# Kernel optimization log

Measured on AMD Instinct MI355X. Metric: run time of the kernel, lower is better.

The kernel has to match this reference:

```python
import jax, jax.numpy as jnp
import numpy as np

N_QUESTIONS = 2000
N_CATS = 4
MEMORY_SIZE = 50
KEY_DIM = 50
VALUE_DIM = 200
FINAL_FC = 50
ABILITY_SCALE = 3.0
BATCH = 1024
SEQ_LEN = 500


def setup_inputs() -> dict:
    key = jax.random.key(0)
    ks = jax.random.split(key, 20)
    f32 = jnp.float32
    inp = {}
    # integer data: question ids in [1, n_questions], responses in [0, K)
    inp['q_data'] = jax.random.randint(ks[0], (BATCH, SEQ_LEN), 1, N_QUESTIONS + 1)
    inp['r_data'] = jax.random.randint(ks[1], (BATCH, SEQ_LEN), 0, N_CATS)
    s = 0.05
    inp['q_embed_w'] = jax.random.normal(ks[2], (N_QUESTIONS + 1, KEY_DIM), f32) * s
    inp['Mk'] = jax.random.normal(ks[3], (MEMORY_SIZE, KEY_DIM), f32) * s
    inp['Mv0'] = jax.random.normal(ks[4], (MEMORY_SIZE, VALUE_DIM), f32) * s
    inp['Wv'] = jax.random.normal(ks[5], (VALUE_DIM, N_CATS * N_QUESTIONS), f32) * s
    inp['bv'] = jnp.zeros((VALUE_DIM,), f32)
    # DKVMN erase / add transforms
    inp['We'] = jax.random.normal(ks[6], (VALUE_DIM, VALUE_DIM), f32) * s
    inp['be'] = jnp.zeros((VALUE_DIM,), f32)
    inp['Wa'] = jax.random.normal(ks[7], (VALUE_DIM, VALUE_DIM), f32) * s
    inp['ba'] = jnp.zeros((VALUE_DIM,), f32)
    # summary network
    inp['Ws'] = jax.random.normal(ks[8], (FINAL_FC, VALUE_DIM + KEY_DIM), f32) * s
    inp['bs'] = jnp.zeros((FINAL_FC,), f32)
    # ability / threshold / discrimination heads
    inp['Wth'] = jax.random.normal(ks[9], (1, FINAL_FC), f32) * s
    inp['bth'] = jnp.zeros((1,), f32)
    inp['Wbeta'] = jax.random.normal(ks[10], (N_CATS - 1, KEY_DIM), f32) * s
    inp['bbeta'] = jnp.zeros((N_CATS - 1,), f32)
    inp['Wdisc'] = jax.random.normal(ks[11], (1, FINAL_FC + KEY_DIM), f32) * s
    inp['bdisc'] = jnp.zeros((1,), f32)
    return inp


def _deep_gpcm(q_data, r_data, q_embed_w, Mk, Mv0, Wv, bv, We, be, Wa, ba,
               Ws, bs, Wth, bth, Wbeta, bbeta, Wdisc, bdisc):
    B, S = q_data.shape
    K = Wbeta.shape[0] + 1
    D = Wv.shape[0]
    Q = Wv.shape[1] // K
    # view gpcm_value_embed weight as (D, K, Q): one-hot(q) @ W == gather column q
    WvK = Wv.reshape(D, K, Q)
    k_idx = jnp.arange(K, dtype=jnp.float32)
    Mv_init = jnp.broadcast_to(Mv0[None], (B,) + Mv0.shape)

    def step(Mv, inp):
        q_t, r_t = inp  # (B,), (B,)
        qe = q_embed_w[q_t]  # (B, key_dim)
        # linear decay weights: max(0, 1 - |k - r| / (K-1))
        w = jnp.maximum(0.0, 1.0 - jnp.abs(k_idx[None, :] - r_t[:, None].astype(jnp.float32)) / (K - 1))  # (B, K)
        Wvq = jnp.take(WvK, q_t - 1, axis=2)  # (D, K, B)
        ve = jnp.einsum('dkb,bk->bd', Wvq, w) + bv  # value embedding (B, D)
        # DKVMN attention + read
        cw = jax.nn.softmax(qe @ Mk.T, axis=-1)  # (B, mem)
        read = jnp.einsum('bm,bmd->bd', cw, Mv)
        # summary / IRT heads
        summary = jnp.tanh(jnp.concatenate([read, qe], axis=-1) @ Ws.T + bs)  # (B, fc)
        theta = ABILITY_SCALE * (summary @ Wth.T + bth)[:, 0]  # (B,)
        betas = jnp.tanh(qe @ Wbeta.T + bbeta)  # (B, K-1)
        alpha = jax.nn.softplus(jnp.concatenate([summary, qe], axis=-1) @ Wdisc.T + bdisc)[:, 0]  # (B,)
        # erase-add memory write
        erase = jax.nn.sigmoid(ve @ We.T + be)
        add = jnp.tanh(ve @ Wa.T + ba)
        Mv_new = Mv * (1.0 - cw[:, :, None] * erase[:, None, :]) + cw[:, :, None] * add[:, None, :]
        # GPCM cumulative logits -> softmax
        cum = jnp.cumsum(alpha[:, None] * (theta[:, None] - betas), axis=-1)  # (B, K-1)
        logits = jnp.concatenate([jnp.zeros((B, 1), cum.dtype), cum], axis=-1)  # (B, K)
        probs = jax.nn.softmax(logits, axis=-1)
        return Mv_new, probs

    _, probs = jax.lax.scan(step, Mv_init, (q_data.T, r_data.T))  # (S, B, K)
    return jnp.transpose(probs, (1, 0, 2))  # (B, S, K)


def reference(q_data, r_data, q_embed_w, Mk, Mv0, Wv, bv, We, be, Wa, ba,
              Ws, bs, Wth, bth, Wbeta, bbeta, Wdisc, bdisc):
    return _deep_gpcm(q_data, r_data, q_embed_w, Mk, Mv0, Wv, bv, We, be, Wa, ba,
                      Ws, bs, Wth, bth, Wbeta, bbeta, Wdisc, bdisc)
```

## Files before the change

kernel.cpp:

```cpp
#include <hip/hip_runtime.h>
#include <hip/hip_bf16.h>
#include <cstdint>
#include <cstddef>


namespace {
constexpr int kB   = 1024;
constexpr int kS   = 500;
constexpr int kQ   = 2000;
constexpr int kKD  = 50;
constexpr int kMem = 50;
constexpr int kD   = 200;
constexpr int kFC  = 50;
constexpr int kWP  = 216;

constexpr size_t OFF_EAD  = 0;
constexpr size_t OFF_CW   = OFF_EAD + (size_t)kQ * 4 * kD * 2;
constexpr size_t OFF_SQ   = OFF_CW + 100064;
constexpr size_t OFF_BQ   = OFF_SQ + 100064;
constexpr size_t OFF_DQ   = OFF_BQ + 8032;
constexpr size_t OFF_CE   = OFF_DQ + 2016;
constexpr size_t OFF_CA   = OFF_CE + 224;
constexpr size_t OFF_WET  = OFF_CA + 224;
constexpr size_t OFF_WAT  = OFF_WET + 40000;
}

typedef float f32x2 __attribute__((ext_vector_type(2)));
typedef _Float16 h2_t __attribute__((ext_vector_type(2)));

__device__ __forceinline__ f32x2 pk_fma(f32x2 a, f32x2 b, f32x2 c) {
  f32x2 d;
  asm("v_pk_fma_f32 %0, %1, %2, %3" : "=v"(d) : "v"(a), "v"(b), "v"(c));
  return d;
}

__device__ __forceinline__ void lds_barrier() {
  asm volatile("s_waitcnt lgkmcnt(0)" ::: "memory");
  __builtin_amdgcn_s_barrier();
  asm volatile("" ::: "memory");
}

__device__ __forceinline__ float fast_tanh(float x) {
  const float ax = fabsf(x);
  const float t = __expf(-2.f * ax);
  const float r = (1.f - t) / (1.f + t);
  return copysignf(r, x);
}
__device__ __forceinline__ float fast_softplus(float x) {
  return fmaxf(x, 0.f) + log1pf(__expf(-fabsf(x)));
}

__global__ void prep1_misc(const float* __restrict__ We, const float* __restrict__ Wa,
                           const float* __restrict__ bv, const float* __restrict__ be,
                           const float* __restrict__ ba, float* __restrict__ ws) {
  float* WeT = ws + OFF_WET;
  float* WaT = ws + OFF_WAT;
  float* ce  = ws + OFF_CE;
  float* ca  = ws + OFF_CA;
  const int gt = blockIdx.x * 256 + threadIdx.x;
  const int stride = gridDim.x * 256;
  for (int e = gt; e < kD * kD; e += stride) {
    const int i = e / kD;
    const int dd = e - i * kD;
    WeT[e] = We[dd * kD + i];
    WaT[e] = Wa[dd * kD + i];
  }
  for (int dd = gt; dd < kD; dd += stride) {
    float acc_e = be[dd], acc_a = ba[dd];
    for (int i = 0; i < kD; ++i) {
      acc_e = fmaf(We[dd * kD + i], bv[i], acc_e);
      acc_a = fmaf(Wa[dd * kD + i], bv[i], acc_a);
    }
    ce[dd] = acc_e;
    ca[dd] = acc_a;
  }
}

__global__ void prep2_ead(const float* __restrict__ Wv, float* __restrict__ ws) {
  __shared__ float s_wv[4][kD];
  const int tid = threadIdx.x;
  const int qm1 = blockIdx.x;
  for (int e = tid; e < 4 * kD; e += 256) {
    const int k = e / kD;
    const int i = e - k * kD;
    s_wv[k][i] = Wv[(size_t)i * (4 * kQ) + (size_t)k * kQ + qm1];
  }
  __syncthreads();
  const int d = tid;
  if (d < kD) {
    const float* WeT = ws + OFF_WET;
    const float* WaT = ws + OFF_WAT;
    float e0 = 0.f, e1 = 0.f, e2 = 0.f, e3 = 0.f;
    float a0 = 0.f, a1 = 0.f, a2 = 0.f, a3 = 0.f;
    for (int i = 0; i < kD; ++i) {
      const float we = WeT[i * kD + d];
      const float wa = WaT[i * kD + d];
      e0 = fmaf(we, s_wv[0][i], e0);
      e1 = fmaf(we, s_wv[1][i], e1);
      e2 = fmaf(we, s_wv[2][i], e2);
      e3 = fmaf(we, s_wv[3][i], e3);
      a0 = fmaf(wa, s_wv[0][i], a0);
      a1 = fmaf(wa, s_wv[1][i], a1);
      a2 = fmaf(wa, s_wv[2][i], a2);
      a3 = fmaf(wa, s_wv[3][i], a3);
    }
    const float ced = ws[OFF_CE + d];
    const float cad = ws[OFF_CA + d];
    const float W[4][4] = {{1.f, 2.f / 3.f, 1.f / 3.f, 0.f},
                           {2.f / 3.f, 1.f, 2.f / 3.f, 1.f / 3.f},
                           {1.f / 3.f, 2.f / 3.f, 1.f, 2.f / 3.f},
                           {0.f, 1.f / 3.f, 2.f / 3.f, 1.f}};
#pragma unroll
    for (int r = 0; r < 4; ++r) {
      const float ep = ced + W[r][0] * e0 + W[r][1] * e1 + W[r][2] * e2 + W[r][3] * e3;
      const float ap = cad + W[r][0] * a0 + W[r][1] * a1 + W[r][2] * a2 + W[r][3] * a3;
      float2 v;
      v.x = 1.f / (1.f + expf(-ep));
      v.y = tanhf(ap);
      *reinterpret_cast<float2*>(ws + OFF_EAD + ((size_t)(qm1 * 4 + r) * kD + d) * 2) = v;
    }
  }
}

__global__ void prep3_qtables(const float* __restrict__ q_embed_w, const float* __restrict__ Mk,
                              const float* __restrict__ Ws, const float* __restrict__ bs,
                              const float* __restrict__ Wbeta, const float* __restrict__ bbeta,
                              const float* __restrict__ Wdisc, float* __restrict__ ws) {
  __shared__ float s_qe[kKD];
  const int tid = threadIdx.x;
  const int q = blockIdx.x;
  if (tid < kKD) s_qe[tid] = q_embed_w[q * kKD + tid];
  __syncthreads();
  {
    float s = -1e30f;
    if (tid < kMem) {
      s = 0.f;
      for (int j = 0; j < kKD; ++j) s = fmaf(s_qe[j], Mk[tid * kKD + j], s);
    }
    float mx = s;
#pragma unroll
    for (int o = 1; o < 64; o <<= 1) mx = fmaxf(mx, __shfl_xor(mx, o));
    const float ev = (tid < kMem) ? expf(s - mx) : 0.f;
    float sm = ev;
#pragma unroll
    for (int o = 1; o < 64; o <<= 1) sm += __shfl_xor(sm, o);
    if (tid < kMem) ws[OFF_CW + (size_t)q * kMem + tid] = ev / sm;
  }
  if (tid < kFC) {
    float s = bs[tid];
    for (int j = 0; j < kKD; ++j) s = fmaf(s_qe[j], Ws[tid * 250 + kD + j], s);
    ws[OFF_SQ + (size_t)q * kFC + tid] = s;
  }
  if (tid < 4) {
    float v = 0.f;
    if (tid < 3) {
      float s = bbeta[tid];
      for (int j = 0; j < kKD; ++j) s = fmaf(s_qe[j], Wbeta[tid * kKD + j], s);
      v = tanhf(s);
    }
    ws[OFF_BQ + (size_t)q * 4 + tid] = v;
  }
  if (tid == 0) {
    float s = 0.f;
    for (int j = 0; j < kKD; ++j) s = fmaf(s_qe[j], Wdisc[kFC + j], s);
    ws[OFF_DQ + q] = s;
  }
}

__device__ __forceinline__ void do_finale(int l, float wth_f, float wds_f, float bth0,
                                          float bdisc0, const float (*s_part)[64],
                                          const float* s_sq_row, const float* s_bqdq_row,
                                          float* out_ptr) {
  float summ = 0.f;
  if (l < kFC) {
    const float sp = s_part[0][l] + s_part[1][l] + s_part[2][l] + s_part[3][l] +
                     s_part[4][l] + s_sq_row[l];
    summ = fast_tanh(sp);
  }
  float p1 = wth_f * summ;
  float p2 = wds_f * summ;
#pragma unroll
  for (int o = 1; o < 64; o <<= 1) {
    p1 += __shfl_xor(p1, o);
    p2 += __shfl_xor(p2, o);
  }
  if (l == 0) {
    const float theta = 3.f * (p1 + bth0);
    const float alpha = fast_softplus(p2 + s_bqdq_row[3] + bdisc0);
    const float c1 = alpha * (theta - s_bqdq_row[0]);
    const float c2 = c1 + alpha * (theta - s_bqdq_row[1]);
    const float c3 = c2 + alpha * (theta - s_bqdq_row[2]);
    const float mx = fmaxf(fmaxf(0.f, c1), fmaxf(c2, c3));
    const float x0 = __expf(0.f - mx);
    const float x1 = __expf(c1 - mx);
    const float x2 = __expf(c2 - mx);
    const float x3 = __expf(c3 - mx);
    const float inv = 1.f / (x0 + x1 + x2 + x3);
    float4 pr;
    pr.x = x0 * inv;
    pr.y = x1 * inv;
    pr.z = x2 * inv;
    pr.w = x3 * inv;
    *reinterpret_cast<float4*>(out_ptr) = pr;
  }
}

__launch_bounds__(256, 4)
__global__ void dkvmn_main(const int* __restrict__ q_data, const int* __restrict__ r_data,
                           const float* __restrict__ Mv0, const float* __restrict__ Ws,
                           const float* __restrict__ Wth, const float* __restrict__ bth,
                           const float* __restrict__ Wdisc, const float* __restrict__ bdisc,
                           const float* __restrict__ ws, float* __restrict__ out) {
  const int tid = threadIdx.x;
  const int b = blockIdx.x;
  const int lane = tid & 63;
  const int wid = tid >> 6;
  const float* EAD = ws + OFF_EAD;
  const float* CW = ws + OFF_CW;
  const float* SQ = ws + OFF_SQ;
  const float* BQ = ws + OFF_BQ;
  const float* DQ = ws + OFF_DQ;

  __shared__ __align__(16) _Float16 s_wsh[kFC * kWP];
  __shared__ __align__(16) _Float16 s_readh[208];
  __shared__ __align__(16) float s_cw[64];
  __shared__ float s_part[5][64];
  __shared__ float s_sq[2][kFC];
  __shared__ float s_bqdq[2][4];
  __shared__ int s_q[kS];
  __shared__ int s_qr[kS];

  for (int e = tid; e < kFC * kD; e += 256) {
    const int f = e / kD;
    const int dd = e - f * kD;
    s_wsh[f * kWP + dd] = (_Float16)Ws[f * 250 + dd];
  }
  {
    const int* qrow = q_data + (size_t)b * kS;
    const int* rrow = r_data + (size_t)b * kS;
    for (int e = tid; e < kS; e += 256) {
      const int qv = qrow[e];
      s_q[e] = qv;
      s_qr[e] = (qv - 1) * 4 + rrow[e];
    }
  }
  f32x2 mv[25];
  const int d = tid;
  const bool dact = (d < kD);
  if (dact) {
#pragma unroll
    for (int m = 0; m < 25; ++m) {
      mv[m][0] = Mv0[(2 * m) * kD + d];
      mv[m][1] = Mv0[(2 * m + 1) * kD + d];
    }
  }
  float wth_f = 0.f, wds_f = 0.f;
  if (wid == 3 && lane < kFC) {
    wth_f = Wth[lane];
    wds_f = Wdisc[lane];
  }
  const float bth0 = bth[0];
  const float bdisc0 = bdisc[0];
  float* out_b = out + (size_t)b * kS * 4;
  __syncthreads();

  const int q0 = s_q[0];
  const int qr0 = s_qr[0];
  float2 ea_cur = make_float2(0.f, 0.f);
  if (dact) ea_cur = *reinterpret_cast<const float2*>(EAD + ((size_t)qr0 * kD + d) * 2);
  float cw_cur = 0.f;
  if (wid == 1 && lane < kMem) cw_cur = CW[(size_t)q0 * kMem + lane];
  float v2_cur = 0.f;
  if (wid == 2) {
    if (lane < kFC) v2_cur = SQ[(size_t)q0 * kFC + lane];
    else if (lane < 53) v2_cur = BQ[(size_t)q0 * 4 + (lane - 50)];
    else if (lane == 53) v2_cur = DQ[q0];
  }

  for (int t = 0; t < kS; ++t) {
    const int pb = t & 1;
    const int tn = (t + 1 < kS) ? (t + 1) : t;
    const int qn = s_q[tn];
    const int qrn = s_qr[tn];
    f32x2 en2 = {0.f, 0.f}, ad2 = {0.f, 0.f};
    float2 ea_nxt = ea_cur;
    if (dact) {
      ea_nxt = *reinterpret_cast<const float2*>(EAD + ((size_t)qrn * kD + d) * 2);
      en2[0] = -ea_cur.x;
      en2[1] = -ea_cur.x;
      ad2[0] = ea_cur.y;
      ad2[1] = ea_cur.y;
    }
    if (wid == 1) {
      if (lane < kMem) {
        s_cw[lane] = cw_cur;
        cw_cur = CW[(size_t)qn * kMem + lane];
      }
    }
    if (wid == 2) {
      if (lane < kFC) {
        s_sq[pb][lane] = v2_cur;
        v2_cur = SQ[(size_t)qn * kFC + lane];
      } else if (lane < 53) {
        s_bqdq[pb][lane - 50] = v2_cur;
        v2_cur = BQ[(size_t)qn * 4 + (lane - 50)];
      } else if (lane == 53) {
        s_bqdq[pb][3] = v2_cur;
        v2_cur = DQ[qn];
      }
    }
    lds_barrier();
    if (dact) {
      f32x2 r2a = {0.f, 0.f}, r2b = {0.f, 0.f};
      const float4* cw4 = reinterpret_cast<const float4*>(s_cw);
#pragma unroll
      for (int g = 0; g < 12; ++g) {
        const float4 c4 = cw4[g];
        const f32x2 clo = {c4.x, c4.y};
        const f32x2 chi = {c4.z, c4.w};
        r2a = pk_fma(clo, mv[2 * g], r2a);
        mv[2 * g] = pk_fma(clo, pk_fma(mv[2 * g], en2, ad2), mv[2 * g]);
        r2b = pk_fma(chi, mv[2 * g + 1], r2b);
        mv[2 * g + 1] = pk_fma(chi, pk_fma(mv[2 * g + 1], en2, ad2), mv[2 * g + 1]);
      }
      {
        const f32x2 clast = *reinterpret_cast<const f32x2*>(&s_cw[48]);
        r2a = pk_fma(clast, mv[24], r2a);
        mv[24] = pk_fma(clast, pk_fma(mv[24], en2, ad2), mv[24]);
      }
      s_readh[d] = (_Float16)((r2a[0] + r2b[0]) + (r2a[1] + r2b[1]));
    }
    if (wid == 3 && t > 0) {
      do_finale(lane, wth_f, wds_f, bth0, bdisc0, s_part, s_sq[pb ^ 1], s_bqdq[pb ^ 1],
                out_b + (size_t)(t - 1) * 4);
    }
    lds_barrier();
    if (tid < 250) {
      const int pc = tid / 50;
      const int pf = tid - pc * 50;
      const float4* wp = reinterpret_cast<const float4*>(s_wsh + pf * kWP + pc * 40);
      const float4* rp = reinterpret_cast<const float4*>(s_readh + pc * 40);
      float acc0 = 0.f, acc1 = 0.f;
#pragma unroll
      for (int g = 0; g < 5; ++g) {
        const float4 wv = wp[g];
        const float4 rv = rp[g];
        acc0 = __builtin_amdgcn_fdot2(__builtin_bit_cast(h2_t, wv.x),
                                      __builtin_bit_cast(h2_t, rv.x), acc0, false);
        acc1 = __builtin_amdgcn_fdot2(__builtin_bit_cast(h2_t, wv.y),
                                      __builtin_bit_cast(h2_t, rv.y), acc1, false);
        acc0 = __builtin_amdgcn_fdot2(__builtin_bit_cast(h2_t, wv.z),
                                      __builtin_bit_cast(h2_t, rv.z), acc0, false);
        acc1 = __builtin_amdgcn_fdot2(__builtin_bit_cast(h2_t, wv.w),
                                      __builtin_bit_cast(h2_t, rv.w), acc1, false);
      }
      s_part[pc][pf] = acc0 + acc1;
    }
    ea_cur = ea_nxt;
  }
  __syncthreads();
  if (wid == 3) {
    do_finale(lane, wth_f, wds_f, bth0, bdisc0, s_part, s_sq[(kS - 1) & 1],
              s_bqdq[(kS - 1) & 1], out_b + (size_t)(kS - 1) * 4);
  }
}

extern "C" void kernel_launch(void* const* d_in, const int* in_sizes, int n_in,
                              void* d_out, int out_size, void* d_ws, size_t ws_size,
                              hipStream_t stream) {
  (void)in_sizes; (void)n_in; (void)out_size; (void)ws_size;
  const int* q_data = (const int*)d_in[0];
  const int* r_data = (const int*)d_in[1];
  const float* q_embed_w = (const float*)d_in[2];
  const float* Mk = (const float*)d_in[3];
  const float* Mv0 = (const float*)d_in[4];
  const float* Wv = (const float*)d_in[5];
  const float* bv = (const float*)d_in[6];
  const float* We = (const float*)d_in[7];
  const float* be = (const float*)d_in[8];
  const float* Wa = (const float*)d_in[9];
  const float* ba = (const float*)d_in[10];
  const float* Ws = (const float*)d_in[11];
  const float* bs = (const float*)d_in[12];
  const float* Wth = (const float*)d_in[13];
  const float* bth = (const float*)d_in[14];
  const float* Wbeta = (const float*)d_in[15];
  const float* bbeta = (const float*)d_in[16];
  const float* Wdisc = (const float*)d_in[17];
  const float* bdisc = (const float*)d_in[18];
  float* out = (float*)d_out;
  float* ws = (float*)d_ws;

  hipLaunchKernelGGL(prep1_misc, dim3(64), dim3(256), 0, stream, We, Wa, bv, be, ba, ws);
  hipLaunchKernelGGL(prep2_ead, dim3(kQ), dim3(256), 0, stream, Wv, ws);
  hipLaunchKernelGGL(prep3_qtables, dim3(kQ + 1), dim3(64), 0, stream, q_embed_w, Mk, Ws, bs,
                     Wbeta, bbeta, Wdisc, ws);
  hipLaunchKernelGGL(dkvmn_main, dim3(kB), dim3(256), 0, stream, q_data, r_data, Mv0, Ws, Wth,
                     bth, Wdisc, bdisc, ws, out);
}
```

Before: 1.389 ms.

## Software-pipeline recurrence stages to use one barrier per timestep

Restructures the per-timestep loop into a three-stage software pipeline. The memory read/update for step t, the summary dot products for step t-1, and the finale for step t-2 run concurrently, using double-buffered cw/read/partial arrays and triple-buffered per-question summary data. This removes one of the two LDS barriers per step, cutting synchronization on the sequential critical path. In exchange it adds an epilogue to drain the pipeline, more shared memory, and more complex buffer index bookkeeping.

```diff
diff --git a/kernel.cpp b/kernel.cpp
--- a/kernel.cpp
+++ b/kernel.cpp
@@ -222,11 +222,11 @@
   const float* DQ = ws + OFF_DQ;
 
   __shared__ __align__(16) _Float16 s_wsh[kFC * kWP];
-  __shared__ __align__(16) _Float16 s_readh[208];
-  __shared__ __align__(16) float s_cw[64];
-  __shared__ float s_part[5][64];
-  __shared__ float s_sq[2][kFC];
-  __shared__ float s_bqdq[2][4];
+  __shared__ __align__(16) _Float16 s_readh[2][208];
+  __shared__ __align__(16) float s_cw[2][64];
+  __shared__ float s_part[2][5][64];
+  __shared__ float s_sq[3][52];
+  __shared__ float s_bqdq[3][4];
   __shared__ int s_q[kS];
   __shared__ int s_qr[kS];
 
@@ -265,54 +265,57 @@
   __syncthreads();
 
   const int q0 = s_q[0];
-  const int qr0 = s_qr[0];
+  const int q1 = s_q[1];
   float2 ea_cur = make_float2(0.f, 0.f);
-  if (dact) ea_cur = *reinterpret_cast<const float2*>(EAD + ((size_t)qr0 * kD + d) * 2);
+  if (dact) ea_cur = *reinterpret_cast<const float2*>(EAD + ((size_t)s_qr[0] * kD + d) * 2);
   float cw_cur = 0.f;
-  if (wid == 1 && lane < kMem) cw_cur = CW[(size_t)q0 * kMem + lane];
+  if (wid == 1 && lane < kMem) {
+    s_cw[0][lane] = CW[(size_t)q0 * kMem + lane];
+    cw_cur = CW[(size_t)q1 * kMem + lane];
+  }
   float v2_cur = 0.f;
   if (wid == 2) {
     if (lane < kFC) v2_cur = SQ[(size_t)q0 * kFC + lane];
     else if (lane < 53) v2_cur = BQ[(size_t)q0 * 4 + (lane - 50)];
     else if (lane == 53) v2_cur = DQ[q0];
   }
-
+  __syncthreads();
+
+  int i3 = 0;
   for (int t = 0; t < kS; ++t) {
     const int pb = t & 1;
-    const int tn = (t + 1 < kS) ? (t + 1) : t;
-    const int qn = s_q[tn];
-    const int qrn = s_qr[tn];
+    const int ip1 = (i3 + 1 < 3) ? i3 + 1 : 0;
+    const int tn1 = (t + 1 < kS) ? t + 1 : kS - 1;
+    const int tn2 = (t + 2 < kS) ? t + 2 : kS - 1;
     f32x2 en2 = {0.f, 0.f}, ad2 = {0.f, 0.f};
     float2 ea_nxt = ea_cur;
     if (dact) {
-      ea_nxt = *reinterpret_cast<const float2*>(EAD + ((size_t)qrn * kD + d) * 2);
+      ea_nxt = *reinterpret_cast<const float2*>(EAD + ((size_t)s_qr[tn1] * kD + d) * 2);
       en2[0] = -ea_cur.x;
       en2[1] = -ea_cur.x;
       ad2[0] = ea_cur.y;
       ad2[1] = ea_cur.y;
     }
-    if (wid == 1) {
-      if (lane < kMem) {
-        s_cw[lane] = cw_cur;
-        cw_cur = CW[(size_t)qn * kMem + lane];
-      }
+    if (wid == 1 && lane < kMem) {
+      s_cw[pb ^ 1][lane] = cw_cur;
+      cw_cur = CW[(size_t)s_q[tn2] * kMem + lane];
     }
     if (wid == 2) {
+      const int qn = s_q[tn1];
       if (lane < kFC) {
-        s_sq[pb][lane] = v2_cur;
+        s_sq[i3][lane] = v2_cur;
         v2_cur = SQ[(size_t)qn * kFC + lane];
       } else if (lane < 53) {
-        s_bqdq[pb][lane - 50] = v2_cur;
+        s_bqdq[i3][lane - 50] = v2_cur;
         v2_cur = BQ[(size_t)qn * 4 + (lane - 50)];
       } else if (lane == 53) {
-        s_bqdq[pb][3] = v2_cur;
+        s_bqdq[i3][3] = v2_cur;
         v2_cur = DQ[qn];
       }
     }
-    lds_barrier();
     if (dact) {
       f32x2 r2a = {0.f, 0.f}, r2b = {0.f, 0.f};
-      const float4* cw4 = reinterpret_cast<const float4*>(s_cw);
+      const float4* cw4 = reinterpret_cast<const float4*>(s_cw[pb]);
 #pragma unroll
       for (int g = 0; g < 12; ++g) {
         const float4 c4 = cw4[g];
@@ -324,22 +327,21 @@
         mv[2 * g + 1] = pk_fma(chi, pk_fma(mv[2 * g + 1], en2, ad2), mv[2 * g + 1]);
       }
       {
-        const f32x2 clast = *reinterpret_cast<const f32x2*>(&s_cw[48]);
+        const f32x2 clast = *reinterpret_cast<const f32x2*>(&s_cw[pb][48]);
         r2a = pk_fma(clast, mv[24], r2a);
         mv[24] = pk_fma(clast, pk_fma(mv[24], en2, ad2), mv[24]);
       }
-      s_readh[d] = (_Float16)((r2a[0] + r2b[0]) + (r2a[1] + r2b[1]));
-    }
-    if (wid == 3 && t > 0) {
-      do_finale(lane, wth_f, wds_f, bth0, bdisc0, s_part, s_sq[pb ^ 1], s_bqdq[pb ^ 1],
-                out_b + (size_t)(t - 1) * 4);
-    }
-    lds_barrier();
+      s_readh[pb][d] = (_Float16)((r2a[0] + r2b[0]) + (r2a[1] + r2b[1]));
+    }
+    if (wid == 3 && t >= 2) {
+      do_finale(lane, wth_f, wds_f, bth0, bdisc0, s_part[pb ^ 1], s_sq[ip1], s_bqdq[ip1],
+                out_b + (size_t)(t - 2) * 4);
+    }
     if (tid < 250) {
       const int pc = tid / 50;
       const int pf = tid - pc * 50;
       const float4* wp = reinterpret_cast<const float4*>(s_wsh + pf * kWP + pc * 40);
-      const float4* rp = reinterpret_cast<const float4*>(s_readh + pc * 40);
+      const float4* rp = reinterpret_cast<const float4*>(&s_readh[pb ^ 1][pc * 40]);
       float acc0 = 0.f, acc1 = 0.f;
 #pragma unroll
       for (int g = 0; g < 5; ++g) {
@@ -354,14 +356,46 @@
         acc1 = __builtin_amdgcn_fdot2(__builtin_bit_cast(h2_t, wv.w),
                                       __builtin_bit_cast(h2_t, rv.w), acc1, false);
       }
-      s_part[pc][pf] = acc0 + acc1;
-    }
+      s_part[pb][pc][pf] = acc0 + acc1;
+    }
+    lds_barrier();
     ea_cur = ea_nxt;
-  }
-  __syncthreads();
-  if (wid == 3) {
-    do_finale(lane, wth_f, wds_f, bth0, bdisc0, s_part, s_sq[(kS - 1) & 1],
-              s_bqdq[(kS - 1) & 1], out_b + (size_t)(kS - 1) * 4);
+    i3 = ip1;
+  }
+  {
+    constexpr int pbE = kS & 1;
+    constexpr int i3a = (kS - 2) % 3;
+    constexpr int i3b = (kS - 1) % 3;
+    if (tid < 250) {
+      const int pc = tid / 50;
+      const int pf = tid - pc * 50;
+      const float4* wp = reinterpret_cast<const float4*>(s_wsh + pf * kWP + pc * 40);
+      const float4* rp = reinterpret_cast<const float4*>(&s_readh[(kS - 1) & 1][pc * 40]);
+      float acc0 = 0.f, acc1 = 0.f;
+#pragma unroll
+      for (int g = 0; g < 5; ++g) {
+        const float4 wv = wp[g];
+        const float4 rv = rp[g];
+        acc0 = __builtin_amdgcn_fdot2(__builtin_bit_cast(h2_t, wv.x),
+                                      __builtin_bit_cast(h2_t, rv.x), acc0, false);
+        acc1 = __builtin_amdgcn_fdot2(__builtin_bit_cast(h2_t, wv.y),
+                                      __builtin_bit_cast(h2_t, rv.y), acc1, false);
+        acc0 = __builtin_amdgcn_fdot2(__builtin_bit_cast(h2_t, wv.z),
+                                      __builtin_bit_cast(h2_t, rv.z), acc0, false);
+        acc1 = __builtin_amdgcn_fdot2(__builtin_bit_cast(h2_t, wv.w),
+                                      __builtin_bit_cast(h2_t, rv.w), acc1, false);
+      }
+      s_part[pbE][pc][pf] = acc0 + acc1;
+    }
+    if (wid == 3) {
+      do_finale(lane, wth_f, wds_f, bth0, bdisc0, s_part[pbE ^ 1], s_sq[i3a], s_bqdq[i3a],
+                out_b + (size_t)(kS - 2) * 4);
+    }
+    lds_barrier();
+    if (wid == 3) {
+      do_finale(lane, wth_f, wds_f, bth0, bdisc0, s_part[pbE], s_sq[i3b], s_bqdq[i3b],
+                out_b + (size_t)(kS - 1) * 4);
+    }
   }
 }
 
```

Result: faster. 1.246 ms (-10.3%).

## Software-pipeline recurrence steps with double-buffered LDS to use one barrier per step

Applied to the files above, without the earlier changes.

Restructures the per-timestep loop into a three-stage software pipeline. The memory update of step t, the summary dot-product of step t-1 and the output finale of step t-2 now run in the same phase. Shared buffers (cw, readh, partials, sq/bqdq) are double- or triple-buffered, which removes one of the two LDS barriers per step, and the loop is unrolled by six with compile-time buffer indices. The cost is more LDS, a deeper prologue and epilogue, and higher register pressure from the unrolling.

```diff
diff --git a/kernel.cpp b/kernel.cpp
--- a/kernel.cpp
+++ b/kernel.cpp
@@ -205,6 +205,80 @@
   }
 }
 
+#define STEP(PB, I3, T, TN1, TN2)                                                     \
+  {                                                                                   \
+    constexpr int IP1_ = ((I3) + 1) % 3;                                              \
+    f32x2 en2 = {0.f, 0.f}, ad2 = {0.f, 0.f};                                         \
+    float2 ea_nxt = ea_cur;                                                           \
+    if (dact) {                                                                       \
+      ea_nxt = EAD2[(size_t)s_qr[(TN1)] * kD + d];                                    \
+      en2[0] = -ea_cur.x;                                                             \
+      en2[1] = -ea_cur.x;                                                             \
+      ad2[0] = ea_cur.y;                                                              \
+      ad2[1] = ea_cur.y;                                                              \
+    }                                                                                 \
+    if (wid == 0 && lane < kMem) {                 \
+      s_cw[(PB) ^ 1][lane] = cw_cur;                                                  \
+      cw_cur = CW[s_q[(TN2)] * kMem + lane];                                          \
+    }                                                                                 \
+    if (wid == 1) {         \
+      const int qn_ = s_q[(TN1)];                                                     \
+      if (lane < kFC) {                                                               \
+        s_sq[(I3)][lane] = v2_cur;                                                    \
+        v2_cur = SQ[qn_ * kFC + lane];                                                \
+      } else if (lane < 53) {                                                         \
+        s_bqdq[(I3)][lane - 50] = v2_cur;                                             \
+        v2_cur = BQ[qn_ * 4 + (lane - 50)];                                           \
+      } else if (lane == 53) {                                                        \
+        s_bqdq[(I3)][3] = v2_cur;                                                     \
+        v2_cur = DQ[qn_];                                                             \
+      }                                                                               \
+    }                                                                                 \
+    if (dact) {                    \
+      f32x2 r2a = {0.f, 0.f}, r2b = {0.f, 0.f};                                       \
+      const float4* cw4_ = reinterpret_cast<const float4*>(s_cw[(PB)]);               \
+      _Pragma("unroll") for (int g = 0; g < 12; ++g) {                                \
+        const float4 c4_ = cw4_[g];                                                   \
+        const f32x2 clo_ = {c4_.x, c4_.y};                                            \
+        const f32x2 chi_ = {c4_.z, c4_.w};                                            \
+        r2a = pk_fma(clo_, mv[2 * g], r2a);                                           \
+        mv[2 * g] = pk_fma(clo_, pk_fma(mv[2 * g], en2, ad2), mv[2 * g]);             \
+        r2b = pk_fma(chi_, mv[2 * g + 1], r2b);                                       \
+        mv[2 * g + 1] = pk_fma(chi_, pk_fma(mv[2 * g + 1], en2, ad2), mv[2 * g + 1]); \
+      }                                                                               \
+      {                                                                               \
+        const f32x2 cl_ = *reinterpret_cast<const f32x2*>(&s_cw[(PB)][48]);           \
+        r2a = pk_fma(cl_, mv[24], r2a);                                               \
+        mv[24] = pk_fma(cl_, pk_fma(mv[24], en2, ad2), mv[24]);                       \
+      }                                                                               \
+      s_readh[(PB)][d] = (_Float16)((r2a[0] + r2b[0]) + (r2a[1] + r2b[1]));           \
+    }                                                                                 \
+    if (wid == 0 && (T) >= 2) {                              \
+      do_finale(lane, wth_f, wds_f, bth0, bdisc0, s_part[(PB) ^ 1], s_sq[IP1_],       \
+                s_bqdq[IP1_], out_b + (size_t)((T) - 2) * 4);                         \
+    }                                                                                 \
+    if (tid < 250) {                    \
+      const float4* wp_ = reinterpret_cast<const float4*>(s_wsh + pf * kWP + pc * 40);\
+      const float4* rp_ = reinterpret_cast<const float4*>(&s_readh[(PB) ^ 1][pc * 40]);\
+      float a0_ = 0.f, a1_ = 0.f;                                                     \
+      _Pragma("unroll") for (int g = 0; g < 5; ++g) {                                 \
+        const float4 wv_ = wp_[g];                                                    \
+        const float4 rv_ = rp_[g];                                                    \
+        a0_ = __builtin_amdgcn_fdot2(__builtin_bit_cast(h2_t, wv_.x),                 \
+                                     __builtin_bit_cast(h2_t, rv_.x), a0_, false);    \
+        a1_ = __builtin_amdgcn_fdot2(__builtin_bit_cast(h2_t, wv_.y),                 \
+                                     __builtin_bit_cast(h2_t, rv_.y), a1_, false);    \
+        a0_ = __builtin_amdgcn_fdot2(__builtin_bit_cast(h2_t, wv_.z),                 \
+                                     __builtin_bit_cast(h2_t, rv_.z), a0_, false);    \
+        a1_ = __builtin_amdgcn_fdot2(__builtin_bit_cast(h2_t, wv_.w),                 \
+                                     __builtin_bit_cast(h2_t, rv_.w), a1_, false);    \
+      }                                                                               \
+      s_part[(PB)][pc][pf] = a0_ + a1_;                                               \
+    }                                                                                 \
+    lds_barrier();                                       \
+    ea_cur = ea_nxt;                                                                  \
+  }
+
 __launch_bounds__(256, 4)
 __global__ void dkvmn_main(const int* __restrict__ q_data, const int* __restrict__ r_data,
                            const float* __restrict__ Mv0, const float* __restrict__ Ws,
@@ -215,18 +289,18 @@
   const int b = blockIdx.x;
   const int lane = tid & 63;
   const int wid = tid >> 6;
-  const float* EAD = ws + OFF_EAD;
+  const float2* EAD2 = reinterpret_cast<const float2*>(ws + OFF_EAD);
   const float* CW = ws + OFF_CW;
   const float* SQ = ws + OFF_SQ;
   const float* BQ = ws + OFF_BQ;
   const float* DQ = ws + OFF_DQ;
 
   __shared__ __align__(16) _Float16 s_wsh[kFC * kWP];
-  __shared__ __align__(16) _Float16 s_readh[208];
-  __shared__ __align__(16) float s_cw[64];
-  __shared__ float s_part[5][64];
-  __shared__ float s_sq[2][kFC];
-  __shared__ float s_bqdq[2][4];
+  __shared__ __align__(16) _Float16 s_readh[2][208];
+  __shared__ __align__(16) float s_cw[2][64];
+  __shared__ float s_part[2][5][64];
+  __shared__ float s_sq[3][52];
+  __shared__ float s_bqdq[3][4];
   __shared__ int s_q[kS];
   __shared__ int s_qr[kS];
 
@@ -244,9 +318,13 @@
       s_qr[e] = (qv - 1) * 4 + rrow[e];
     }
   }
-  f32x2 mv[25];
   const int d = tid;
   const bool dact = (d < kD);
+  const int pc = tid / 50;
+  const int pf = tid - pc * 50;
+  f32x2 mv[25];
+#pragma unroll
+  for (int m = 0; m < 25; ++m) mv[m] = f32x2{0.f, 0.f};
   if (dact) {
 #pragma unroll
     for (int m = 0; m < 25; ++m) {
@@ -255,7 +333,7 @@
     }
   }
   float wth_f = 0.f, wds_f = 0.f;
-  if (wid == 3 && lane < kFC) {
+  if (wid == 0 && lane < kFC) {
     wth_f = Wth[lane];
     wds_f = Wdisc[lane];
   }
@@ -265,81 +343,41 @@
   __syncthreads();
 
   const int q0 = s_q[0];
-  const int qr0 = s_qr[0];
+  const int q1 = s_q[1];
   float2 ea_cur = make_float2(0.f, 0.f);
-  if (dact) ea_cur = *reinterpret_cast<const float2*>(EAD + ((size_t)qr0 * kD + d) * 2);
+  if (dact) ea_cur = EAD2[(size_t)s_qr[0] * kD + d];
   float cw_cur = 0.f;
-  if (wid == 1 && lane < kMem) cw_cur = CW[(size_t)q0 * kMem + lane];
+  if (wid == 0 && lane < kMem) {
+    s_cw[0][lane] = CW[q0 * kMem + lane];
+    cw_cur = CW[q1 * kMem + lane];
+  }
   float v2_cur = 0.f;
-  if (wid == 2) {
-    if (lane < kFC) v2_cur = SQ[(size_t)q0 * kFC + lane];
-    else if (lane < 53) v2_cur = BQ[(size_t)q0 * 4 + (lane - 50)];
+  if (wid == 1) {
+    if (lane < kFC) v2_cur = SQ[q0 * kFC + lane];
+    else if (lane < 53) v2_cur = BQ[q0 * 4 + (lane - 50)];
     else if (lane == 53) v2_cur = DQ[q0];
   }
-
-  for (int t = 0; t < kS; ++t) {
-    const int pb = t & 1;
-    const int tn = (t + 1 < kS) ? (t + 1) : t;
-    const int qn = s_q[tn];
-    const int qrn = s_qr[tn];
-    f32x2 en2 = {0.f, 0.f}, ad2 = {0.f, 0.f};
-    float2 ea_nxt = ea_cur;
-    if (dact) {
-      ea_nxt = *reinterpret_cast<const float2*>(EAD + ((size_t)qrn * kD + d) * 2);
-      en2[0] = -ea_cur.x;
-      en2[1] = -ea_cur.x;
-      ad2[0] = ea_cur.y;
-      ad2[1] = ea_cur.y;
-    }
-    if (wid == 1) {
-      if (lane < kMem) {
-        s_cw[lane] = cw_cur;
-        cw_cur = CW[(size_t)qn * kMem + lane];
-      }
-    }
-    if (wid == 2) {
-      if (lane < kFC) {
-        s_sq[pb][lane] = v2_cur;
-        v2_cur = SQ[(size_t)qn * kFC + lane];
-      } else if (lane < 53) {
-        s_bqdq[pb][lane - 50] = v2_cur;
-        v2_cur = BQ[(size_t)qn * 4 + (lane - 50)];
-      } else if (lane == 53) {
-        s_bqdq[pb][3] = v2_cur;
-        v2_cur = DQ[qn];
-      }
-    }
-    lds_barrier();
-    if (dact) {
-      f32x2 r2a = {0.f, 0.f}, r2b = {0.f, 0.f};
-      const float4* cw4 = reinterpret_cast<const float4*>(s_cw);
-#pragma unroll
-      for (int g = 0; g < 12; ++g) {
-        const float4 c4 = cw4[g];
-        const f32x2 clo = {c4.x, c4.y};
-        const f32x2 chi = {c4.z, c4.w};
-        r2a = pk_fma(clo, mv[2 * g], r2a);
-        mv[2 * g] = pk_fma(clo, pk_fma(mv[2 * g], en2, ad2), mv[2 * g]);
-        r2b = pk_fma(chi, mv[2 * g + 1], r2b);
-        mv[2 * g + 1] = pk_fma(chi, pk_fma(mv[2 * g + 1], en2, ad2), mv[2 * g + 1]);
-      }
-      {
-        const f32x2 clast = *reinterpret_cast<const f32x2*>(&s_cw[48]);
-        r2a = pk_fma(clast, mv[24], r2a);
-        mv[24] = pk_fma(clast, pk_fma(mv[24], en2, ad2), mv[24]);
-      }
-      s_readh[d] = (_Float16)((r2a[0] + r2b[0]) + (r2a[1] + r2b[1]));
-    }
-    if (wid == 3 && t > 0) {
-      do_finale(lane, wth_f, wds_f, bth0, bdisc0, s_part, s_sq[pb ^ 1], s_bqdq[pb ^ 1],
-                out_b + (size_t)(t - 1) * 4);
-    }
-    lds_barrier();
+  __syncthreads();
+
+  for (int it = 0; it < 83; ++it) {
+    const int t0 = 6 * it;
+    STEP(0, 0, t0 + 0, t0 + 1, t0 + 2)
+    STEP(1, 1, t0 + 1, t0 + 2, t0 + 3)
+    STEP(0, 2, t0 + 2, t0 + 3, t0 + 4)
+    STEP(1, 0, t0 + 3, t0 + 4, t0 + 5)
+    STEP(0, 1, t0 + 4, t0 + 5, t0 + 6)
+    STEP(1, 2, t0 + 5, t0 + 6, t0 + 7)
+  }
+  STEP(0, 0, 498, 499, 499)
+  STEP(1, 1, 499, 499, 499)
+
+  {
+    constexpr int pbE = kS & 1;
+    constexpr int i3a = (kS - 2) % 3;
+    constexpr int i3b = (kS - 1) % 3;
     if (tid < 250) {
-      const int pc = tid / 50;
-      const int pf = tid - pc * 50;
       const float4* wp = reinterpret_cast<const float4*>(s_wsh + pf * kWP + pc * 40);
-      const float4* rp = reinterpret_cast<const float4*>(s_readh + pc * 40);
+      const float4* rp = reinterpret_cast<const float4*>(&s_readh[(kS - 1) & 1][pc * 40]);
       float acc0 = 0.f, acc1 = 0.f;
 #pragma unroll
       for (int g = 0; g < 5; ++g) {
@@ -354,14 +392,17 @@
         acc1 = __builtin_amdgcn_fdot2(__builtin_bit_cast(h2_t, wv.w),
                                       __builtin_bit_cast(h2_t, rv.w), acc1, false);
       }
-      s_part[pc][pf] = acc0 + acc1;
-    }
-    ea_cur = ea_nxt;
-  }
-  __syncthreads();
-  if (wid == 3) {
-    do_finale(lane, wth_f, wds_f, bth0, bdisc0, s_part, s_sq[(kS - 1) & 1],
-              s_bqdq[(kS - 1) & 1], out_b + (size_t)(kS - 1) * 4);
+      s_part[pbE][pc][pf] = acc0 + acc1;
+    }
+    if (wid == 0) {
+      do_finale(lane, wth_f, wds_f, bth0, bdisc0, s_part[pbE ^ 1], s_sq[i3a], s_bqdq[i3a],
+                out_b + (size_t)(kS - 2) * 4);
+    }
+    lds_barrier();
+    if (wid == 0) {
+      do_finale(lane, wth_f, wds_f, bth0, bdisc0, s_part[pbE], s_sq[i3b], s_bqdq[i3b],
+                out_b + (size_t)(kS - 1) * 4);
+    }
   }
 }
 
```

Result: faster. 1.266 ms (-8.9%).
